# Optimization experiments

Hardware: AMD Instinct MI355X
Metric: run time of the kernel (lower is better)

The kernel has to match this reference:

```python
import jax, jax.numpy as jnp
import numpy as np
from jax import lax

B, P, GRID, NP = 16, 220, 4, 16
DIM, DEPTH, HEADS, DH, MLP, NC = 512, 6, 8, 64, 2048, 1000
EPS = 1e-5
SCALE = DH ** -0.5
FLAT = 64 * 16 * 16  # per-patch CNN output [64,16,16] flattened (c,p1,p2 order)


def setup_inputs() -> dict:
    key = jax.random.key(0)
    ks = iter(jax.random.split(key, 40))
    def n(shape, std):
        return jax.random.normal(next(ks), shape, dtype=jnp.float32) * std
    return {
        "img": jax.random.normal(next(ks), (B, 1, GRID * P, GRID * P), dtype=jnp.float32),
        "conv1_w": n((32, 1, 7, 7), (2.0 / 49) ** 0.5),
        "conv2_w": n((64, 32, 7, 7), (2.0 / (32 * 49)) ** 0.5),
        "conv3_w": n((64, 64, 7, 7), (2.0 / (64 * 49)) ** 0.5),
        "flat_w": n((FLAT, DIM), FLAT ** -0.5),
        "flat_b": jnp.zeros((DIM,), jnp.float32),
        "cls_token": n((1, 1, DIM), 0.02),
        "pos_emb": n((1, NP + 1, DIM), 0.02),
        "ln1_g": jnp.ones((DEPTH, DIM), jnp.float32),
        "ln1_b": jnp.zeros((DEPTH, DIM), jnp.float32),
        "qkv_w": n((DEPTH, DIM, 3 * HEADS * DH), DIM ** -0.5),
        "out_w": n((DEPTH, HEADS * DH, DIM), (HEADS * DH) ** -0.5),
        "out_b": jnp.zeros((DEPTH, DIM), jnp.float32),
        "ln2_g": jnp.ones((DEPTH, DIM), jnp.float32),
        "ln2_b": jnp.zeros((DEPTH, DIM), jnp.float32),
        "ff1_w": n((DEPTH, DIM, MLP), DIM ** -0.5),
        "ff1_b": jnp.zeros((DEPTH, MLP), jnp.float32),
        "ff2_w": n((DEPTH, MLP, DIM), MLP ** -0.5),
        "ff2_b": jnp.zeros((DEPTH, DIM), jnp.float32),
        "head_ln_g": jnp.ones((DIM,), jnp.float32),
        "head_ln_b": jnp.zeros((DIM,), jnp.float32),
        "head_w": n((DIM, NC), DIM ** -0.5),
        "head_b": jnp.zeros((NC,), jnp.float32),
    }


def _ln(x, g, b):
    m = jnp.mean(x, axis=-1, keepdims=True)
    v = jnp.mean(jnp.square(x - m), axis=-1, keepdims=True)
    return (x - m) * lax.rsqrt(v + EPS) * g + b


def _cnn(x, w1, w2, w3):
    def block(h, w):
        h = lax.conv_general_dilated(h, w, (2, 2), 'VALID',
                                     dimension_numbers=('NCHW', 'OIHW', 'NCHW'))
        h = jax.nn.relu(h)
        # MaxPool2d(kernel=7, stride=1, padding=1)
        return lax.reduce_window(h, -jnp.inf, lax.max, (1, 1, 7, 7), (1, 1, 1, 1),
                                 ((0, 0), (0, 0), (1, 1), (1, 1)))
    return block(block(block(x, w1), w2), w3)


def _forward(img, conv1_w, conv2_w, conv3_w, flat_w, flat_b, cls_token, pos_emb,
             ln1_g, ln1_b, qkv_w, out_w, out_b, ln2_g, ln2_b,
             ff1_w, ff1_b, ff2_w, ff2_b, head_ln_g, head_ln_b, head_w, head_b):
    # b c (h p1) (w p2) -> (b h w) 1 p1 p2 ; all patches batched through the CNN at once
    patches = img.reshape(B, 1, GRID, P, GRID, P).transpose(0, 2, 4, 3, 1, 5)
    patches = patches.reshape(B * NP, 1, P, P)
    feat = _cnn(patches, conv1_w, conv2_w, conv3_w).reshape(B, NP, FLAT)  # [B,NP,64*16*16]
    x = feat @ flat_w + flat_b                                            # [B,NP,DIM]
    x = jnp.concatenate([jnp.broadcast_to(cls_token, (B, 1, DIM)), x], axis=1) + pos_emb
    N = NP + 1

    def layer(x, p):
        g1, b1, qw, ow, ob, g2, b2, w1, fb1, w2, fb2 = p
        h = _ln(x, g1, b1)
        q, k, v = jnp.split(h @ qw, 3, axis=-1)
        def heads(t):
            return t.reshape(B, N, HEADS, DH).transpose(0, 2, 1, 3)  # b h n d
        q, k, v = heads(q), heads(k), heads(v)
        attn = jax.nn.softmax(jnp.einsum('bhqd,bhkd->bhqk', q, k) * SCALE, axis=-1)
        o = jnp.einsum('bhqk,bhkd->bhqd', attn, v).transpose(0, 2, 1, 3).reshape(B, N, HEADS * DH)
        x = x + o @ ow + ob
        h2 = _ln(x, g2, b2)
        x = x + jax.nn.gelu(h2 @ w1 + fb1, approximate=False) @ w2 + fb2
        return x, None

    x, _ = lax.scan(layer, x, (ln1_g, ln1_b, qkv_w, out_w, out_b,
                               ln2_g, ln2_b, ff1_w, ff1_b, ff2_w, ff2_b))
    cls = _ln(x[:, 0], head_ln_g, head_ln_b)
    return cls @ head_w + head_b  # [B, NC]


def reference(img, conv1_w, conv2_w, conv3_w, flat_w, flat_b, cls_token, pos_emb,
              ln1_g, ln1_b, qkv_w, out_w, out_b, ln2_g, ln2_b,
              ff1_w, ff1_b, ff2_w, ff2_b, head_ln_g, head_ln_b, head_w, head_b):
    return _forward(img, conv1_w, conv2_w, conv3_w, flat_w, flat_b, cls_token, pos_emb,
                    ln1_g, ln1_b, qkv_w, out_w, out_b, ln2_g, ln2_b,
                    ff1_w, ff1_b, ff2_w, ff2_b, head_ln_g, head_ln_b, head_w, head_b)
```

## Files before the change

kernel.cpp:

```cpp
#include <hip/hip_runtime.h>
#include <hip/hip_bf16.h>


typedef __hip_bfloat16 bf16;
typedef __attribute__((ext_vector_type(8))) short short8;
typedef __attribute__((ext_vector_type(4))) float floatx4;

#define CHUNK 64

union U8 { int4 v; unsigned short s[8]; };
__device__ inline void umax8(U8& a, const U8& b){
  #pragma unroll
  for (int j = 0; j < 8; j++) a.s[j] = (a.s[j] > b.s[j]) ? a.s[j] : b.s[j];
}
union U4 { uint2 v; unsigned short s[4]; };
__device__ inline void umax4(U4& a, const U4& b){
  #pragma unroll
  for (int j = 0; j < 4; j++) a.s[j] = (a.s[j] > b.s[j]) ? a.s[j] : b.s[j];
}

__global__ __launch_bounds__(256) void prep_w2(const float* __restrict__ w,
                                               bf16* __restrict__ w2b)
{
  int idx = blockIdx.x*256 + threadIdx.x;
  if (idx >= 49*64*32) return;
  int ic = idx & 31; int t = idx >> 5; int oc = t & 63; int kk = t >> 6;
  int ky = kk/7, kx = kk - ky*7;
  w2b[idx] = __float2bfloat16(w[((oc*32+ic)*7+ky)*7+kx]);
}

__global__ __launch_bounds__(256) void prep_w3(const float* __restrict__ w,
                                               bf16* __restrict__ w3b)
{
  int idx = blockIdx.x*256 + threadIdx.x;
  if (idx >= 49*2*64*32) return;
  int ic_l = idx & 31; int t = idx >> 5; int oc = t & 63; int t2 = t >> 6;
  int kx = t2 % 7; int t3 = t2 / 7; int kc = t3 & 1; int ky = t3 >> 1;
  w3b[idx] = __float2bfloat16(w[((oc*64 + kc*32 + ic_l)*7+ky)*7+kx]);
}

__global__ __launch_bounds__(256) void prep_pack(
    const float* __restrict__ src, bf16* __restrict__ dst,
    int K8, int N, int total)
{
  int idx = blockIdx.x*256 + threadIdx.x;
  if (idx >= total) return;
  int n = idx % N; int t = idx / N; int k8 = t % K8; int l = t / K8;
  const float* s = src + ((size_t)l*K8*8 + (size_t)k8*8)*N + n;
  union { bf16 h[8]; int4 v; } pk;
  #pragma unroll
  for (int j = 0; j < 8; j++) pk.h[j] = __float2bfloat16(s[(size_t)j*N]);
  *(int4*)(dst + (((size_t)l*K8 + k8)*N + n)*8) = pk.v;
}

__global__ __launch_bounds__(256) void prep_pack_flat(
    const float* __restrict__ src, bf16* __restrict__ hi, bf16* __restrict__ lo)
{
  int idx = blockIdx.x*256 + threadIdx.x;
  if (idx >= 2048*512) return;
  int n = idx & 511; int k8 = idx >> 9;
  const float* s = src + (size_t)k8*8*512 + n;
  union { bf16 h[8]; int4 v; } ph, pl;
  #pragma unroll
  for (int j = 0; j < 8; j++){
    float w = s[(size_t)j*512];
    bf16 h = __float2bfloat16(w);
    ph.h[j] = h;
    pl.h[j] = __float2bfloat16(w - __bfloat162float(h));
  }
  size_t o = (size_t)idx*8;
  *(int4*)(hi + o) = ph.v;
  *(int4*)(lo + o) = pl.v;
}

__global__ __launch_bounds__(256) void k1a_conv1(
    const float* __restrict__ img, const float* __restrict__ w,
    bf16* __restrict__ cbuf, int n_base)
{
  __shared__ __align__(16) float in_s[15*224];
  __shared__ float w_s[32*58];
  const int band = blockIdx.x;
  const int n = blockIdx.y;
  const int ng = n_base + n;
  const int r0 = band*5;
  const int ir0 = 2*r0;
  const int b = ng>>4, gh = (ng>>2)&3, gw = ng&3;
  const float* ibase = img + b*774400 + (gh*220)*880 + gw*220;

  for (int idx = threadIdx.x; idx < 15*56; idx += 256){
    int r = idx/56, cq = idx - r*56; int c = cq*4;
    int gr = ir0 + r;
    float4 v = (c < 220 && gr < 220) ? *(const float4*)(ibase + gr*880 + c)
                                     : make_float4(0.f,0.f,0.f,0.f);
    *(float4*)&in_s[r*224 + c] = v;
  }
  for (int idx = threadIdx.x; idx < 32*56; idx += 256){
    int oc = idx/56, k = idx - oc*56; int ky = k>>3, kx = k&7;
    w_s[oc*58 + k] = (kx < 7) ? w[oc*49 + ky*7 + kx] : 0.f;
  }
  __syncthreads();

  const int grp = threadIdx.x & 7;
  const int sp  = threadIdx.x >> 3;
  const int cgc = (sp < 26) ? sp : 26;
  const int nrows = (107 - r0 < 5) ? (107 - r0) : 5;

  float acc[5][4][4] = {};
  #pragma unroll 1
  for (int ky = 0; ky < 7; ky++){
    float wk[4][7];
    #pragma unroll
    for (int oc = 0; oc < 4; oc++)
      #pragma unroll
      for (int kx = 0; kx < 7; kx++)
        wk[oc][kx] = w_s[(grp*4+oc)*58 + ky*8 + kx];
    #pragma unroll
    for (int i = 0; i < 5; i++){
      if (i < nrows){
        const float* ip = &in_s[(2*i+ky)*224 + 8*cgc];
        float iv[13];
        *(float4*)&iv[0] = *(const float4*)ip;
        *(float4*)&iv[4] = *(const float4*)(ip+4);
        *(float4*)&iv[8] = *(const float4*)(ip+8);
        iv[12] = ip[12];
        #pragma unroll
        for (int oc = 0; oc < 4; oc++)
          #pragma unroll
          for (int kx = 0; kx < 7; kx++)
            #pragma unroll
            for (int j = 0; j < 4; j++)
              acc[i][oc][j] += iv[2*j+kx]*wk[oc][kx];
      }
    }
  }

  #pragma unroll
  for (int i = 0; i < 5; i++){
    if (i < nrows){
      int y = r0 + i;
      #pragma unroll
      for (int j = 0; j < 4; j++){
        int col = 4*sp + j;
        if (col < 107){
          union { unsigned short s[4]; uint2 u; } pk;
          #pragma unroll
          for (int oc = 0; oc < 4; oc++){
            bf16 hv = __float2bfloat16(fmaxf(acc[i][oc][j], 0.f));
            pk.s[oc] = *(unsigned short*)&hv;
          }
          *(uint2*)(cbuf + (((size_t)(n*8+grp)*107 + y)*107 + col)*4) = pk.u;
        }
      }
    }
  }
}

__global__ __launch_bounds__(256) void k1b_pool1(
    const bf16* __restrict__ cbuf, bf16* __restrict__ pool1, int n_pool_base)
{
  __shared__ uint2 in4[19*107];
  __shared__ uint2 ht4[19*103];
  const int s = blockIdx.x, g = blockIdx.y, n = blockIdx.z;
  const int p0 = s*13;
  const int PR = (103 - p0 < 13) ? (103 - p0) : 13;
  const int NR = PR + 6;
  const uint2* src = (const uint2*)cbuf + (size_t)(n*8+g)*107*107;

  for (int t = threadIdx.x; t < NR*107; t += 256){
    int r = t/107, c = t - r*107;
    int gr = p0 - 1 + r;
    gr = (gr < 0) ? 0 : ((gr > 106) ? 106 : gr);
    in4[t] = src[gr*107 + c];
  }
  __syncthreads();
  for (int t = threadIdx.x; t < NR*103; t += 256){
    int r = t/103, c = t - r*103;
    U4 m; m.v = in4[r*107 + ((c > 0) ? c-1 : 0)];
    #pragma unroll
    for (int d = 0; d < 6; d++){
      U4 v; v.v = in4[r*107 + ((c+d < 106) ? c+d : 106)];
      umax4(m, v);
    }
    ht4[r*103 + c] = m.v;
  }
  __syncthreads();
  uint2* dst = (uint2*)pool1;
  const size_t plane = ((size_t)(n_pool_base + n)*4 + (g>>1))*10609;
  const int h = g & 1;
  for (int t = threadIdx.x; t < PR*103; t += 256){
    int pr = t/103, c = t - pr*103;
    U4 m; m.v = ht4[pr*103 + c];
    #pragma unroll
    for (int d = 1; d < 7; d++){
      U4 v; v.v = ht4[(pr+d)*103 + c];
      umax4(m, v);
    }
    dst[(plane + (size_t)(p0+pr)*103 + c)*2 + h] = m.v;
  }
}

__global__ __launch_bounds__(256) void k2_conv2(
    const bf16* __restrict__ pool1,
    const bf16* __restrict__ w2b,
    bf16* __restrict__ conv2out)
{
  __shared__ __align__(16) bf16 in_s[7*2*52*36];
  const int n = blockIdx.y, pb = blockIdx.x;
  const int wv = threadIdx.x >> 6, lane = threadIdx.x & 63;
  const int li = lane & 15, lg = lane >> 4;
  const int p0 = pb*256;
  const int y0 = p0/49;

  int pyv[4], pxv[4]; bool pmask[4];
  #pragma unroll
  for (int t = 0; t < 4; t++){
    int p = p0 + wv*64 + t*16 + li;
    pmask[t] = (p <= 2400);
    int pc = min(p, 2400);
    int yy = pc/49, xx = pc - yy*49;
    pyv[t] = yy; pxv[t] = xx;
  }
  floatx4 acc[4][4];
  #pragma unroll
  for (int a = 0; a < 4; a++)
    #pragma unroll
    for (int t = 0; t < 4; t++) acc[a][t] = (floatx4){0.f,0.f,0.f,0.f};

  const unsigned short* pbase = (const unsigned short*)pool1;

  auto stage_rows = [&](int e0, int cnt, int par){
    for (int idx = threadIdx.x; idx < cnt*103*4; idx += 256){
      int q = idx & 3; int t2 = idx >> 2; int ri = t2/103; int c = t2 - ri*103;
      int e = e0 + ri;
      int slot = e % 7;
      int gr = min(2*e + par, 102);
      *(int4*)&in_s[((slot*2 + (c&1))*52 + (c>>1))*36 + q*8] =
        *(const int4*)(pbase + (((size_t)n*4 + q)*10609 + (size_t)gr*103 + c)*8);
    }
  };

  const int kyseq[7] = {0,2,4,6,1,3,5};
  #pragma unroll 1
  for (int ks = 0; ks < 7; ks++){
    int ky = kyseq[ks];
    int kyh = ky >> 1, par = ky & 1;
    __syncthreads();
    if (ks == 0 || ks == 4) stage_rows(y0, 7, par);
    else                    stage_rows(y0 + 6 + kyh, 1, par);
    __syncthreads();
    int poff[4];
    #pragma unroll
    for (int t = 0; t < 4; t++){
      int e = pyv[t] + kyh;
      int slot = e % 7;
      poff[t] = (slot*2*52 + pxv[t])*36;
    }
    #pragma unroll
    for (int kx = 0; kx < 7; kx++){
      short8 a[4];
      const bf16* wp = w2b + (ky*7+kx)*64*32;
      #pragma unroll
      for (int ot = 0; ot < 4; ot++)
        a[ot] = *(const short8*)(wp + (ot*16 + li)*32 + lg*8);
      int koff = ((kx&1)*52 + (kx>>1))*36 + lg*8;
      #pragma unroll
      for (int t = 0; t < 4; t++){
        short8 bfr = *(const short8*)(&in_s[poff[t] + koff]);
        #pragma unroll
        for (int ot = 0; ot < 4; ot++)
          acc[ot][t] = __builtin_amdgcn_mfma_f32_16x16x32_bf16(a[ot], bfr, acc[ot][t], 0, 0, 0);
      }
    }
  }
  #pragma unroll
  for (int t = 0; t < 4; t++){
    if (!pmask[t]) continue;
    bf16* dst = conv2out + (((long)n*49 + pyv[t])*49 + pxv[t])*64 + lg*4;
    #pragma unroll
    for (int ot = 0; ot < 4; ot++){
      union { bf16 h[4]; uint2 u; } pk;
      #pragma unroll
      for (int v = 0; v < 4; v++)
        pk.h[v] = __float2bfloat16(fmaxf(acc[ot][t][v], 0.f));
      *(uint2*)(dst + ot*16) = pk.u;
    }
  }
}

__global__ __launch_bounds__(256) void k3a_hmax(
    const bf16* __restrict__ cin, bf16* __restrict__ tmp)
{
  int idx = blockIdx.x*256 + threadIdx.x;
  int cg = idx & 7; int t = idx >> 3; int x = t % 45; int t2 = t / 45;
  int y = t2 % 49; int n = t2 / 49;
  const int4* row = (const int4*)(cin + ((long)(n*49 + y)*49)*64) + cg;
  U8 m; m.v = make_int4(0,0,0,0);
  int lo = max(x-1, 0), hi = min(x+5, 48);
  for (int cx = lo; cx <= hi; cx++){ U8 v; v.v = row[cx*8]; umax8(m, v); }
  *((int4*)(tmp + ((long)(n*49 + y)*45 + x)*64) + cg) = m.v;
}

__global__ __launch_bounds__(256) void k3b_vmax(
    const bf16* __restrict__ tmp, bf16* __restrict__ pout, int n_base)
{
  int idx = blockIdx.x*256 + threadIdx.x;
  int cg = idx & 7; int t = idx >> 3; int x = t % 45; int t2 = t / 45;
  int y = t2 % 45; int n = t2 / 45;
  U8 m; m.v = make_int4(0,0,0,0);
  int lo = max(y-1, 0), hi = min(y+5, 48);
  for (int cy = lo; cy <= hi; cy++){
    U8 v; v.v = *((const int4*)(tmp + ((long)(n*49 + cy)*45 + x)*64) + cg);
    umax8(m, v);
  }
  *((int4*)(pout + (long)(n_base+n)*129600 + (y*45 + x)*64) + cg) = m.v;
}

__global__ __launch_bounds__(256) void k4_conv3(
    const bf16* __restrict__ pool2,
    const bf16* __restrict__ w3b,
    bf16* __restrict__ conv3out)
{
  __shared__ __align__(16) bf16 in_s[10*2*24*40];
  const int n = blockIdx.y, pb = blockIdx.x;
  const int wv = threadIdx.x >> 6, lane = threadIdx.x & 63;
  const int li = lane & 15, lg = lane >> 4;
  const int y0 = pb*10;

  int pyv[4], pxv[4], poff[4]; bool pmask[4];
  #pragma unroll
  for (int t = 0; t < 4; t++){
    int pl = wv*64 + t*16 + li;
    pmask[t] = (pl < 200);
    int p = pb*200 + min(pl, 199);
    int yy = p/20, xx = p - yy*20;
    pyv[t] = yy; pxv[t] = xx;
    poff[t] = ((yy - y0)*2*24 + xx)*40;
  }
  floatx4 acc[4][4];
  #pragma unroll
  for (int a = 0; a < 4; a++)
    #pragma unroll
    for (int t = 0; t < 4; t++) acc[a][t] = (floatx4){0.f,0.f,0.f,0.f};

  for (int ky = 0; ky < 7; ky++){
    for (int kc = 0; kc < 2; kc++){
      __syncthreads();
      for (int idx = threadIdx.x; idx < 10*45*4; idx += 256){
        int q = idx & 3; int t2 = idx >> 2; int c = t2 % 45; int r = t2/45;
        int gr = 2*(y0+r)+ky;
        const bf16* src = pool2 + (((long)n*45 + gr)*45 + c)*64 + kc*32 + q*8;
        bf16* dst = &in_s[((r*2 + (c&1))*24 + (c>>1))*40 + q*8];
        *(int4*)dst = *(const int4*)src;
      }
      __syncthreads();
      #pragma unroll
      for (int kx = 0; kx < 7; kx++){
        short8 a[4];
        const bf16* wp = w3b + ((ky*2+kc)*7 + kx)*64*32;
        #pragma unroll
        for (int ot = 0; ot < 4; ot++)
          a[ot] = *(const short8*)(wp + (ot*16 + li)*32 + lg*8);
        int koff = ((kx&1)*24 + (kx>>1))*40 + lg*8;
        #pragma unroll
        for (int t = 0; t < 4; t++){
          short8 bfr = *(const short8*)(&in_s[poff[t] + koff]);
          #pragma unroll
          for (int ot = 0; ot < 4; ot++)
            acc[ot][t] = __builtin_amdgcn_mfma_f32_16x16x32_bf16(a[ot], bfr, acc[ot][t], 0, 0, 0);
        }
      }
    }
  }
  #pragma unroll
  for (int t = 0; t < 4; t++){
    if (!pmask[t]) continue;
    bf16* dst = conv3out + (((long)n*20 + pyv[t])*20 + pxv[t])*64 + lg*4;
    #pragma unroll
    for (int ot = 0; ot < 4; ot++){
      union { bf16 h[4]; uint2 u; } pk;
      #pragma unroll
      for (int v = 0; v < 4; v++)
        pk.h[v] = __float2bfloat16(fmaxf(acc[ot][t][v], 0.f));
      *(uint2*)(dst + ot*16) = pk.u;
    }
  }
}

__global__ __launch_bounds__(256) void k5_pool3(
    const bf16* __restrict__ cin, bf16* __restrict__ feat)
{
  __shared__ int4 in_p[3200];
  __shared__ int4 ht[2560];
  const int n = blockIdx.x;
  const int4* src = (const int4*)(cin + (long)n*25600);
  for (int i = threadIdx.x; i < 3200; i += 256) in_p[i] = src[i];
  __syncthreads();
  for (int i = threadIdx.x; i < 2560; i += 256){
    int cg = i & 7; int t = i >> 3; int x = t & 15; int y = t >> 4;
    U8 m; m.v = make_int4(0,0,0,0);
    int lo = max(x-1, 0), hi = min(x+5, 19);
    for (int cx = lo; cx <= hi; cx++){ U8 v; v.v = in_p[(y*20+cx)*8 + cg]; umax8(m, v); }
    ht[(y*16+x)*8 + cg] = m.v;
  }
  __syncthreads();
  unsigned short* dst = (unsigned short*)(feat + (long)n*16384);
  for (int i = threadIdx.x; i < 2048; i += 256){
    int px = i & 15; int py = (i >> 4) & 15; int cg = i >> 8;
    U8 m; m.v = make_int4(0,0,0,0);
    int lo = max(py-1, 0), hi = min(py+5, 19);
    for (int cy = lo; cy <= hi; cy++){ U8 v; v.v = ht[(cy*16+px)*8 + cg]; umax8(m, v); }
    #pragma unroll
    for (int j = 0; j < 8; j++)
      dst[(cg*8+j)*256 + py*16 + px] = m.s[j];
  }
}

__global__ __launch_bounds__(256) void k6_init_x(
    const float* __restrict__ cls, const float* __restrict__ pos,
    const float* __restrict__ flat_b, float* __restrict__ x)
{
  int idx = blockIdx.x*256 + threadIdx.x;
  int d = idx & 511; int row = idx >> 9;
  int tt = row % 17;
  x[idx] = (tt == 0) ? (cls[d] + pos[d]) : (flat_b[d] + pos[tt*512 + d]);
}

__global__ __launch_bounds__(256) void k6_flat_mfma(
    const bf16* __restrict__ feat, const bf16* __restrict__ Whi,
    const bf16* __restrict__ Wlo, float* __restrict__ x)
{
  const int wv = threadIdx.x >> 6, lane = threadIdx.x & 63;
  const int li = lane & 15, lg = lane >> 4;
  const int m0 = blockIdx.x*64 + wv*16;
  const int nb = blockIdx.y*64;
  const int kb = blockIdx.z*2048;
  floatx4 acc[4];
  #pragma unroll
  for (int t = 0; t < 4; t++) acc[t] = (floatx4){0.f,0.f,0.f,0.f};

  const bf16* arow = feat + (size_t)(m0+li)*16384 + kb + lg*8;
  for (int k0 = 0; k0 < 2048; k0 += 32){
    short8 a = *(const short8*)(arow + k0);
    size_t wo = ((size_t)((kb + k0) >> 3) + lg)*512 + nb + li;
    const bf16* wh = Whi + wo*8;
    const bf16* wl = Wlo + wo*8;
    #pragma unroll
    for (int t = 0; t < 4; t++){
      short8 bh = *(const short8*)(wh + t*128);
      acc[t] = __builtin_amdgcn_mfma_f32_16x16x32_bf16(a, bh, acc[t], 0, 0, 0);
    }
    #pragma unroll
    for (int t = 0; t < 4; t++){
      short8 bl = *(const short8*)(wl + t*128);
      acc[t] = __builtin_amdgcn_mfma_f32_16x16x32_bf16(a, bl, acc[t], 0, 0, 0);
    }
  }
  #pragma unroll
  for (int t = 0; t < 4; t++){
    int col = nb + t*16 + li;
    #pragma unroll
    for (int v = 0; v < 4; v++){
      int m = m0 + lg*4 + v;
      int row = (m>>4)*17 + 1 + (m&15);
      atomicAdd(&x[row*512 + col], acc[t][v]);
    }
  }
}

__global__ __launch_bounds__(256) void ln_kernel(
    const float* __restrict__ in, const float* __restrict__ g,
    const float* __restrict__ b, float* __restrict__ out,
    int in_stride, int out_stride)
{
  int row = blockIdx.x;
  const float* p = in + (long)row*in_stride;
  float v0 = p[threadIdx.x], v1 = p[threadIdx.x+256];
  __shared__ float red[4]; __shared__ float stat;
  float s = v0+v1;
  #pragma unroll
  for (int o = 32; o >= 1; o >>= 1) s += __shfl_down(s, o);
  int lane = threadIdx.x & 63, wv = threadIdx.x >> 6;
  if (lane == 0) red[wv] = s;
  __syncthreads();
  if (threadIdx.x == 0) stat = (red[0]+red[1]+red[2]+red[3])*(1.0f/512.0f);
  __syncthreads();
  float m = stat;
  float d0 = v0-m, d1 = v1-m;
  float q = d0*d0 + d1*d1;
  #pragma unroll
  for (int o = 32; o >= 1; o >>= 1) q += __shfl_down(q, o);
  __syncthreads();
  if (lane == 0) red[wv] = q;
  __syncthreads();
  if (threadIdx.x == 0) stat = rsqrtf((red[0]+red[1]+red[2]+red[3])*(1.0f/512.0f) + 1e-5f);
  __syncthreads();
  float rstd = stat;
  out[(long)row*out_stride + threadIdx.x]     = d0*rstd*g[threadIdx.x]     + b[threadIdx.x];
  out[(long)row*out_stride + threadIdx.x+256] = d1*rstd*g[threadIdx.x+256] + b[threadIdx.x+256];
}

__global__ __launch_bounds__(256) void ln_bf16(
    const float* __restrict__ in, const float* __restrict__ g,
    const float* __restrict__ b, bf16* __restrict__ out)
{
  int row = blockIdx.x;
  const float* p = in + (long)row*512;
  float v0 = p[threadIdx.x], v1 = p[threadIdx.x+256];
  __shared__ float red[4]; __shared__ float stat;
  float s = v0+v1;
  #pragma unroll
  for (int o = 32; o >= 1; o >>= 1) s += __shfl_down(s, o);
  int lane = threadIdx.x & 63, wv = threadIdx.x >> 6;
  if (lane == 0) red[wv] = s;
  __syncthreads();
  if (threadIdx.x == 0) stat = (red[0]+red[1]+red[2]+red[3])*(1.0f/512.0f);
  __syncthreads();
  float m = stat;
  float d0 = v0-m, d1 = v1-m;
  float q = d0*d0 + d1*d1;
  #pragma unroll
  for (int o = 32; o >= 1; o >>= 1) q += __shfl_down(q, o);
  __syncthreads();
  if (lane == 0) red[wv] = q;
  __syncthreads();
  if (threadIdx.x == 0) stat = rsqrtf((red[0]+red[1]+red[2]+red[3])*(1.0f/512.0f) + 1e-5f);
  __syncthreads();
  float rstd = stat;
  out[(long)row*512 + threadIdx.x]     = __float2bfloat16(d0*rstd*g[threadIdx.x]     + b[threadIdx.x]);
  out[(long)row*512 + threadIdx.x+256] = __float2bfloat16(d1*rstd*g[threadIdx.x+256] + b[threadIdx.x+256]);
}

template<int NT>
__global__ __launch_bounds__(256) void tail_gemm(
    const bf16* __restrict__ A, const bf16* __restrict__ Wp,
    const float* __restrict__ bias, const float* res,
    float* outf, bf16* outb, int N, int K, int dogelu)
{
  const int wv = threadIdx.x >> 6, lane = threadIdx.x & 63;
  const int li = lane & 15, lg = lane >> 4;
  const int m0 = blockIdx.x * 16;
  const int nb = blockIdx.y * (64*NT) + wv * (16*NT);
  floatx4 acc[NT];
  #pragma unroll
  for (int t = 0; t < NT; t++) acc[t] = (floatx4){0.f,0.f,0.f,0.f};
  const bf16* arow = A + (size_t)(m0+li)*K + lg*8;
  for (int k0 = 0; k0 < K; k0 += 32){
    short8 a = *(const short8*)(arow + k0);
    const bf16* wrow = Wp + ((size_t)((k0>>3) + lg) * N + nb + li) * 8;
    #pragma unroll
    for (int t = 0; t < NT; t++){
      short8 bfr = *(const short8*)(wrow + t*128);
      acc[t] = __builtin_amdgcn_mfma_f32_16x16x32_bf16(a, bfr, acc[t], 0, 0, 0);
    }
  }
  #pragma unroll
  for (int t = 0; t < NT; t++){
    int col = nb + t*16 + li;
    #pragma unroll
    for (int v = 0; v < 4; v++){
      int row = m0 + lg*4 + v;
      float val = acc[t][v];
      if (bias) val += bias[col];
      if (dogelu) val = 0.5f*val*(1.0f + erff(val*0.70710678118654752f));
      if (res) val += res[(size_t)row*N + col];
      if (outf) outf[(size_t)row*N + col] = val;
      else      outb[(size_t)row*N + col] = __float2bfloat16(val);
    }
  }
}

__global__ __launch_bounds__(256) void gemm_rows(
    const float* __restrict__ A, const float* __restrict__ W,
    const float* __restrict__ bias, const float* __restrict__ res,
    float* __restrict__ out, int M, int N, int K, int dogelu)
{
  __shared__ float A_s[16][33];
  __shared__ __align__(16) float W_s[32][68];
  const int m0 = blockIdx.x*16, n0 = blockIdx.y*64;
  const int r = threadIdx.x>>4, c0 = (threadIdx.x&15)*4;
  float acc[4] = {};
  for (int k0 = 0; k0 < K; k0 += 32){
    __syncthreads();
    for (int i = 0; i < 2; i++){ int id = threadIdx.x + i*256; int rr = id>>5, kk = id&31;
      A_s[rr][kk] = (m0+rr < M) ? A[(long)(m0+rr)*K + k0+kk] : 0.f; }
    for (int i = 0; i < 8; i++){ int id = threadIdx.x + i*256; int kk = id>>6, c = id&63;
      W_s[kk][c] = (n0+c < N) ? W[(long)(k0+kk)*N + n0+c] : 0.f; }
    __syncthreads();
    #pragma unroll
    for (int kk = 0; kk < 32; kk++){
      float a = A_s[r][kk];
      float4 w4 = *(const float4*)&W_s[kk][c0];
      acc[0]+=a*w4.x; acc[1]+=a*w4.y; acc[2]+=a*w4.z; acc[3]+=a*w4.w;
    }
  }
  if (m0+r < M){
    int row = m0+r;
    for (int j = 0; j < 4; j++){
      int c = n0+c0+j;
      if (c < N){
        float v = acc[j];
        if (bias) v += bias[c];
        if (dogelu) v = 0.5f*v*(1.0f + erff(v*0.70710678118654752f));
        if (res) v += res[(long)row*N + c];
        out[(long)row*N + c] = v;
      }
    }
  }
}

__global__ __launch_bounds__(128) void attn_kernel(
    const float* __restrict__ qkv, bf16* __restrict__ obuf)
{
  const int b = blockIdx.x >> 3, h = blockIdx.x & 7;
  __shared__ float q_s[17][65], k_s[17][65], v_s[17][65], s_s[17][18];
  for (int idx = threadIdx.x; idx < 17*64; idx += 128){
    int i = idx>>6, d = idx&63;
    const float* base = qkv + (long)(b*17+i)*1536 + h*64 + d;
    q_s[i][d] = base[0]; k_s[i][d] = base[512]; v_s[i][d] = base[1024];
  }
  __syncthreads();
  for (int idx = threadIdx.x; idx < 289; idx += 128){
    int i = idx/17, j = idx - i*17;
    float s = 0.f;
    for (int d = 0; d < 64; d++) s += q_s[i][d]*k_s[j][d];
    s_s[i][j] = s*0.125f;
  }
  __syncthreads();
  if (threadIdx.x < 17){
    int i = threadIdx.x;
    float m = -1e30f;
    for (int j = 0; j < 17; j++) m = fmaxf(m, s_s[i][j]);
    float sum = 0.f;
    for (int j = 0; j < 17; j++){ float e = expf(s_s[i][j]-m); s_s[i][j] = e; sum += e; }
    float inv = 1.0f/sum;
    for (int j = 0; j < 17; j++) s_s[i][j] *= inv;
  }
  __syncthreads();
  for (int idx = threadIdx.x; idx < 17*64; idx += 128){
    int i = idx>>6, d = idx&63;
    float o = 0.f;
    for (int j = 0; j < 17; j++) o += s_s[i][j]*v_s[j][d];
    obuf[(long)(b*17+i)*512 + h*64 + d] = __float2bfloat16(o);
  }
}

extern "C" void kernel_launch(void* const* d_in, const int* in_sizes, int n_in,
                              void* d_out, int out_size, void* d_ws, size_t ws_size,
                              hipStream_t stream) {
  const float* img      = (const float*)d_in[0];
  const float* conv1_w  = (const float*)d_in[1];
  const float* conv2_w  = (const float*)d_in[2];
  const float* conv3_w  = (const float*)d_in[3];
  const float* flat_w   = (const float*)d_in[4];
  const float* flat_b   = (const float*)d_in[5];
  const float* cls_tok  = (const float*)d_in[6];
  const float* pos_emb  = (const float*)d_in[7];
  const float* ln1_g    = (const float*)d_in[8];
  const float* ln1_b    = (const float*)d_in[9];
  const float* qkv_w    = (const float*)d_in[10];
  const float* out_w    = (const float*)d_in[11];
  const float* out_b    = (const float*)d_in[12];
  const float* ln2_g    = (const float*)d_in[13];
  const float* ln2_b    = (const float*)d_in[14];
  const float* ff1_w    = (const float*)d_in[15];
  const float* ff1_b    = (const float*)d_in[16];
  const float* ff2_w    = (const float*)d_in[17];
  const float* ff2_b    = (const float*)d_in[18];
  const float* hln_g    = (const float*)d_in[19];
  const float* hln_b    = (const float*)d_in[20];
  const float* head_w   = (const float*)d_in[21];
  const float* head_b   = (const float*)d_in[22];

  char* ws = (char*)d_ws;
  size_t off = 0;
  auto alloc = [&](size_t bytes) -> void* {
    void* p = ws + off; off += (bytes + 255) & ~(size_t)255; return p;
  };
  bf16* pool1    = (bf16*)alloc((size_t)CHUNK*8*103*103*4*2);
  bf16* conv2out = (bf16*)alloc((size_t)CHUNK*49*49*64*2);
  bf16* pool2    = (bf16*)alloc((size_t)256*45*45*64*2);
  bf16* feat     = (bf16*)alloc((size_t)256*16384*2);
  bf16* w2b      = (bf16*)alloc((size_t)49*64*32*2);
  bf16* w3b      = (bf16*)alloc((size_t)49*2*64*32*2);
  float* x       = (float*)alloc((size_t)139264*4);
  bf16*  hb      = (bf16*)alloc((size_t)139264*2);
  float* qkvb    = (float*)alloc((size_t)417792*4);
  bf16*  obufb   = (bf16*)alloc((size_t)139264*2);
  bf16*  ffbufb  = (bf16*)alloc((size_t)557056*2);
  float* hcls    = (float*)alloc((size_t)8192*4);
  bf16* tmp3     = pool1;
  bf16* conv3out = pool1;
  bf16* qkvp  = pool1;
  bf16* outwp = qkvp  + (size_t)6*512*1536;
  bf16* ff1p  = outwp + (size_t)6*512*512;
  bf16* ff2p  = ff1p  + (size_t)6*512*2048;
  bf16* fwhi  = conv2out;
  bf16* fwlo  = pool2;

  const size_t cb_per_n = (size_t)8*107*107*4*2;
  int SUB; bf16* cbuf;
  if (ws_size >= off + 64*cb_per_n)      { SUB = 64; cbuf = (bf16*)alloc(64*cb_per_n); }
  else if (ws_size >= off + 32*cb_per_n) { SUB = 32; cbuf = (bf16*)alloc(32*cb_per_n); }
  else { SUB = 16; cbuf = conv2out; }
  (void)in_sizes; (void)n_in; (void)out_size;

  prep_w2<<<392, 256, 0, stream>>>(conv2_w, w2b);
  prep_w3<<<784, 256, 0, stream>>>(conv3_w, w3b);

  for (int cb = 0; cb < 256; cb += CHUNK){
    for (int sb = 0; sb < CHUNK; sb += SUB){
      k1a_conv1<<<dim3(22, SUB), 256, 0, stream>>>(img, conv1_w, cbuf, cb + sb);
      k1b_pool1<<<dim3(8, 8, SUB), 256, 0, stream>>>(cbuf, pool1, sb);
    }
    k2_conv2     <<<dim3(10,CHUNK), 256, 0, stream>>>(pool1, w2b, conv2out);
    k3a_hmax     <<<(CHUNK*49*45*8)/256, 256, 0, stream>>>(conv2out, tmp3);
    k3b_vmax     <<<(CHUNK*45*45*8)/256, 256, 0, stream>>>(tmp3, pool2, cb);
  }
  k4_conv3<<<dim3(2,256), 256, 0, stream>>>(pool2, w3b, conv3out);
  k5_pool3<<<256, 256, 0, stream>>>(conv3out, feat);

  prep_pack_flat<<<4096, 256, 0, stream>>>(flat_w, fwhi, fwlo);
  prep_pack<<<(6*64*1536+255)/256, 256, 0, stream>>>(qkv_w, qkvp, 64, 1536, 6*64*1536);
  prep_pack<<<(6*64*512 +255)/256, 256, 0, stream>>>(out_w, outwp, 64, 512,  6*64*512);
  prep_pack<<<(6*64*2048+255)/256, 256, 0, stream>>>(ff1_w, ff1p, 64, 2048, 6*64*2048);
  prep_pack<<<(6*256*512+255)/256, 256, 0, stream>>>(ff2_w, ff2p, 256, 512, 6*256*512);

  k6_init_x    <<<544,         256, 0, stream>>>(cls_tok, pos_emb, flat_b, x);
  k6_flat_mfma <<<dim3(4,8,8), 256, 0, stream>>>(feat, fwhi, fwlo, x);

  for (int l = 0; l < 6; l++){
    ln_bf16<<<272, 256, 0, stream>>>(x, ln1_g + l*512, ln1_b + l*512, hb);
    tail_gemm<4><<<dim3(17,6), 256, 0, stream>>>(hb, qkvp + (size_t)l*786432,
                                                 nullptr, nullptr, qkvb, nullptr, 1536, 512, 0);
    attn_kernel<<<128, 128, 0, stream>>>(qkvb, obufb);
    tail_gemm<1><<<dim3(17,8), 256, 0, stream>>>(obufb, outwp + (size_t)l*262144,
                                                 out_b + l*512, x, x, nullptr, 512, 512, 0);
    ln_bf16<<<272, 256, 0, stream>>>(x, ln2_g + l*512, ln2_b + l*512, hb);
    tail_gemm<4><<<dim3(17,8), 256, 0, stream>>>(hb, ff1p + (size_t)l*1048576,
                                                 ff1_b + l*2048, nullptr, nullptr, ffbufb, 2048, 512, 1);
    tail_gemm<1><<<dim3(17,8), 256, 0, stream>>>(ffbufb, ff2p + (size_t)l*1048576,
                                                 ff2_b + l*512, x, x, nullptr, 512, 2048, 0);
  }

  ln_kernel<<<16, 256, 0, stream>>>(x, hln_g, hln_b, hcls, 17*512, 512);
  gemm_rows<<<dim3(1,16), 256, 0, stream>>>(hcls, head_w, head_b, nullptr,
                                            (float*)d_out, 16, 1000, 512, 0);
}
```

Measured before the change: 1.599 ms.

## Reuse staged input rows across ky via ring buffer in conv3

Reorders the conv3 kernel-row loop so even and odd ky values are processed in sequence, letting consecutive ky share nine of the ten staged input rows. The shared buffer becomes a ring indexed modulo 10, and only one new row is loaded per step instead of all ten. This cuts global-to-LDS traffic for the conv3 input, at the cost of modulo indexing and a less unrolled loop nest.

```diff
diff --git a/kernel.cpp b/kernel.cpp
--- a/kernel.cpp
+++ b/kernel.cpp
@@ -326,7 +326,7 @@
   const int li = lane & 15, lg = lane >> 4;
   const int y0 = pb*10;
 
-  int pyv[4], pxv[4], poff[4]; bool pmask[4];
+  int pyv[4], pxv[4]; bool pmask[4];
   #pragma unroll
   for (int t = 0; t < 4; t++){
     int pl = wv*64 + t*16 + li;
@@ -334,7 +334,6 @@
     int p = pb*200 + min(pl, 199);
     int yy = p/20, xx = p - yy*20;
     pyv[t] = yy; pxv[t] = xx;
-    poff[t] = ((yy - y0)*2*24 + xx)*40;
   }
   floatx4 acc[4][4];
   #pragma unroll
@@ -342,17 +341,35 @@
     #pragma unroll
     for (int t = 0; t < 4; t++) acc[a][t] = (floatx4){0.f,0.f,0.f,0.f};
 
-  for (int ky = 0; ky < 7; ky++){
-    for (int kc = 0; kc < 2; kc++){
+  auto stage_rows = [&](int e0, int cnt, int par, int kc){
+    for (int idx = threadIdx.x; idx < cnt*45*4; idx += 256){
+      int q = idx & 3; int t2 = idx >> 2; int ri = t2/45; int c = t2 - ri*45;
+      int e = e0 + ri;
+      int slot = e % 10;
+      int gr = 2*e + par;
+      *(int4*)&in_s[((slot*2 + (c&1))*24 + (c>>1))*40 + q*8] =
+        *(const int4*)(pool2 + (((long)n*45 + gr)*45 + c)*64 + kc*32 + q*8);
+    }
+  };
+
+  const int kyseq[7] = {0,2,4,6,1,3,5};
+  #pragma unroll 1
+  for (int kc = 0; kc < 2; kc++){
+    #pragma unroll 1
+    for (int ks = 0; ks < 7; ks++){
+      int ky = kyseq[ks];
+      int kyh = ky >> 1, par = ky & 1;
       __syncthreads();
-      for (int idx = threadIdx.x; idx < 10*45*4; idx += 256){
-        int q = idx & 3; int t2 = idx >> 2; int c = t2 % 45; int r = t2/45;
-        int gr = 2*(y0+r)+ky;
-        const bf16* src = pool2 + (((long)n*45 + gr)*45 + c)*64 + kc*32 + q*8;
-        bf16* dst = &in_s[((r*2 + (c&1))*24 + (c>>1))*40 + q*8];
-        *(int4*)dst = *(const int4*)src;
+      if (ks == 0 || ks == 4) stage_rows(y0 + kyh, 10, par, kc);
+      else                    stage_rows(y0 + 9 + kyh, 1, par, kc);
+      __syncthreads();
+      int poff[4];
+      #pragma unroll
+      for (int t = 0; t < 4; t++){
+        int e = pyv[t] + kyh;
+        int slot = e % 10;
+        poff[t] = (slot*2*24 + pxv[t])*40;
       }
-      __syncthreads();
       #pragma unroll
       for (int kx = 0; kx < 7; kx++){
         short8 a[4];
```

After: 1.578 ms. No clear change (-1.3%).
